# Optimization experiments

Measured on AMD Instinct MI355X. Metric: run time of the kernel, lower is better.

## Reference

```python
import jax, jax.numpy as jnp
import numpy as np
import itertools, math
from collections import Counter

# ----- circuit / state constants -----
M = 12            # modes
NPH = 5           # photons (input_state = [1]*5 + [0]*7)
NTHETA = 12       # trainable phase shifters
NX = 8            # input phase shifters (input_size)
NPARAMS = NTHETA + NX
OUT = 10
TWO_PI = 2.0 * np.pi

# all output Fock states with NPH photons in M modes, as sorted row-index multisets
ROW_IDX = np.array(list(itertools.combinations_with_replacement(range(M), NPH)), np.int32)  # [S, NPH]
S = ROW_IDX.shape[0]  # C(M+NPH-1, NPH) = 4368
# normalization prod(s_j!) for each output state (input state is 0/1 so its factor is 1)
NORM = np.array([np.prod([math.factorial(v) for v in Counter(tuple(r)).values()]) for r in ROW_IDX], np.float32)

# Ryser subsets of the NPH columns
K = 1 << NPH
MASKS = np.array([[(s >> j) & 1 for j in range(NPH)] for s in range(K)], np.float32)  # [K, NPH]
SIGNS = ((-1.0) ** (MASKS.sum(1) + NPH)).astype(np.float32)                            # [K]

# fixed 50/50 beamsplitter layers (perceval BS convention: 1/sqrt2 [[1, i],[i, 1]])
def _bs_layer(pairs):
    Bm = np.eye(M, dtype=np.complex64)
    r = np.float32(1.0 / np.sqrt(2.0))
    for (i, j) in pairs:
        Bm[i, i] = r; Bm[j, j] = r
        Bm[i, j] = 1j * r; Bm[j, i] = 1j * r
    return Bm
BS_EVEN = _bs_layer([(i, i + 1) for i in range(0, M - 1, 2)])
BS_ODD = _bs_layer([(i, i + 1) for i in range(1, M - 1, 2)])


def build_unitaries(x, thetas):
    """x: [B, NX] in [0,1]; thetas: [NTHETA]. Returns batched unitaries [B, M, M] complex64."""
    b = x.shape[0]
    phis = jnp.concatenate([jnp.broadcast_to(thetas, (b, NTHETA)), x * TWO_PI], axis=1)  # [B, NPARAMS]
    U = jnp.broadcast_to(jnp.eye(M, dtype=jnp.complex64), (b, M, M))
    for k in range(NPARAMS):
        mode = k % M
        phase = jnp.exp(1j * phis[:, k])  # [B] complex64
        ph = jnp.ones((b, M), jnp.complex64).at[:, mode].set(phase)
        U = ph[:, :, None] * U                               # apply phase shifter (diag @ U)
        Bm = jnp.asarray(BS_EVEN if k % 2 == 0 else BS_ODD)
        U = jnp.einsum('ij,bjk->bik', Bm, U)                 # apply BS layer
    return U


def slos_distribution(U):
    """Boson-sampling output distribution: p(s) = |perm(U[s_rows, :NPH])|^2 / prod(s_j!)."""
    Ucols = U[:, :, :NPH]  # photons enter modes 0..NPH-1 -> keep those columns, [B, M, NPH]
    masks = jnp.asarray(MASKS).astype(jnp.complex64)
    signs = jnp.asarray(SIGNS).astype(jnp.complex64)
    row_idx = jnp.asarray(ROW_IDX)

    def body(acc, ms):
        mask, sign = ms
        rs = Ucols @ mask              # row sums over subset columns, [B, M]
        rows = rs[:, row_idx]          # gather rows per output state, [B, S, NPH]
        return acc + sign * jnp.prod(rows, axis=-1), None

    acc0 = jnp.zeros((U.shape[0], S), jnp.complex64)
    perm, _ = jax.lax.scan(jax.checkpoint(body), acc0, (masks, signs))  # Ryser over 2^NPH subsets
    probs = (perm.real ** 2 + perm.imag ** 2) / jnp.asarray(NORM)
    return probs  # [B, S]


def setup_inputs() -> dict:
    key = jax.random.key(0)
    k1, k2, k3 = jax.random.split(key, 3)
    x = jax.random.uniform(k1, (512, NX), dtype=jnp.float32)                 # inputs in [0,1]
    thetas = jax.random.uniform(k2, (NTHETA,), dtype=jnp.float32) * np.pi    # init in [0, pi]
    W = jax.random.normal(k3, (S, OUT), dtype=jnp.float32) / np.sqrt(S)      # linear output mapping
    b = jnp.zeros((OUT,), jnp.float32)
    return {"x": x, "thetas": thetas, "W": W, "b": b}


def reference(x, thetas, W, b):
    U = build_unitaries(x, thetas)
    probs = slos_distribution(U)
    return probs @ W + b  # [B, OUT]
```

## Files before the change

kernel.cpp:

```cpp
#include <hip/hip_runtime.h>


#define MODES 12
#define NPH   5
#define KG    16
#define QG    8
#define NPAIR 78
#define S_TOT 4368
#define TPB   512
#define NWAVE (TPB / 64)
#define NOUT  10
#define NENT  720

#define TWO_PI_F 6.28318530717958647692f
#define RS2      0.70710678118654752440f

constexpr int Cnk(int n, int r) {
  int p = 1;
  for (int i = 0; i < r; ++i) p = p * (n - i) / (i + 1);
  return p;
}

struct Tables {
  unsigned       ea[NENT];
  unsigned       eb[NENT];
  unsigned char  wr[NENT];
  unsigned short cstart[TPB + 1];
  unsigned char  pairs[NPAIR];
};

constexpr Tables make_tables() {
  Tables T{};
  int ne = 0;
  for (int v = 11; v >= 0; --v) {
    unsigned P[364] = {};
    int cnt = 0;
    for (int m0 = 0; m0 <= v; ++m0)
      for (int m1 = m0; m1 <= v; ++m1)
        for (int m2 = m1; m2 <= v; ++m2) {
          int sbase = 0;
          for (int q = 0;  q < m0; ++q) sbase += Cnk(15 - q, 4);
          for (int q = m0; q < m1; ++q) sbase += Cnk(14 - q, 3);
          for (int q = m1; q < m2; ++q) sbase += Cnk(13 - q, 2);
          for (int q = m2; q < v;  ++q) sbase += 12 - q;
          int r1 = 1, pm = 1;
          r1 = (m1 == m0) ? r1 + 1 : 1; pm *= r1;
          r1 = (m2 == m1) ? r1 + 1 : 1; pm *= r1;
          r1 = (v  == m2) ? r1 + 1 : 1; pm *= r1;
          int code = 0;
          if (pm == 1)       code = 0;
          else if (pm == 2)  code = (r1 == 1) ? 1 : 2;
          else if (pm == 4)  code = 3;
          else if (pm == 6)  code = (r1 == 1) ? 4 : 5;
          else               code = 6;
          P[cnt++] = ((unsigned)code << 29) | ((unsigned)sbase << 16) |
                     ((unsigned)m0 << 12) | ((unsigned)m1 << 8) |
                     ((unsigned)m2 << 4) | (unsigned)v;
        }
    const int np = (cnt + 1) / 2;
    for (int j = 0; j < np; ++j) {
      unsigned a = P[2 * j];
      unsigned b = (2 * j + 1 < cnt) ? P[2 * j + 1] : a;
      if (v <= 4) {
        int mid = (v + 12) / 2;
        T.ea[ne] = a; T.eb[ne] = b; T.wr[ne] = (unsigned char)((v << 4) | mid);  ne++;
        T.ea[ne] = a; T.eb[ne] = b; T.wr[ne] = (unsigned char)((mid << 4) | 12); ne++;
      } else {
        T.ea[ne] = a; T.eb[ne] = b; T.wr[ne] = (unsigned char)((v << 4) | 12);   ne++;
      }
    }
  }
  long total = 0;
  for (int i = 0; i < NENT; ++i)
    total += 32 + 8 * ((T.wr[i] & 15) - (T.wr[i] >> 4));
  long cum = 0;
  int ci = 0;
  T.cstart[0] = 0;
  for (int i = 0; i < NENT; ++i) {
    cum += 32 + 8 * ((T.wr[i] & 15) - (T.wr[i] >> 4));
    while (ci < TPB - 1 && cum * TPB >= (long)(ci + 1) * total)
      T.cstart[++ci] = (unsigned short)(i + 1);
  }
  while (ci < TPB) T.cstart[++ci] = NENT;
  int pi = 0;
  for (int a = 0; a < MODES; ++a)
    for (int b = a; b < MODES; ++b)
      T.pairs[pi++] = (unsigned char)((a << 4) | b);
  return T;
}

__constant__ Tables g_tab = make_tables();

__constant__ float2 g_normlut[7] = {
  {1.f / 512.f,   1.f / 256.f},
  {1.f / 1024.f,  1.f / 512.f},
  {1.f / 1536.f,  1.f / 512.f},
  {1.f / 3072.f,  1.f / 1024.f},
  {1.f / 3072.f,  1.f / 1536.f},
  {1.f / 6144.f,  1.f / 1536.f},
  {1.f / 30720.f, 1.f / 6144.f},
};

#define BFLY(i, j)                                                 \
  { float ar = ur[i], ai = ui[i], br = ur[j], bi = ui[j];          \
    ur[i] = RS2 * (ar - bi); ui[i] = RS2 * (ai + br);              \
    ur[j] = RS2 * (br - ai); ui[j] = RS2 * (bi + ar); }

#define PREFA(q)                                                    \
  { float4 A = ppt[q][p01a], B = ppt[q][p2va];                      \
    pf##q = make_float4(A.x*B.x - A.y*B.y, A.x*B.y + A.y*B.x,       \
                        A.z*B.z - A.w*B.w, A.z*B.w + A.w*B.z); }
#define PREFB(q)                                                    \
  { float4 A = ppt[q][p01b], B = ppt[q][p2vb];                      \
    pg##q = make_float4(A.x*B.x - A.y*B.y, A.x*B.y + A.y*B.x,       \
                        A.z*B.z - A.w*B.w, A.z*B.w + A.w*B.z); }

#define WSTEP2(q, PRA, PIA, PRB, PIB)                                   \
  { float4 e2 = rsp[q][w];                                              \
    PRA = fmaf(pf##q.x, e2.x, PRA); PRA = fmaf(-pf##q.y, e2.y, PRA);    \
    PIA = fmaf(pf##q.x, e2.y, PIA); PIA = fmaf(pf##q.y, e2.x, PIA);     \
    PRA = fmaf(pf##q.z, e2.z, PRA); PRA = fmaf(-pf##q.w, e2.w, PRA);    \
    PIA = fmaf(pf##q.z, e2.w, PIA); PIA = fmaf(pf##q.w, e2.z, PIA);     \
    PRB = fmaf(pg##q.x, e2.x, PRB); PRB = fmaf(-pg##q.y, e2.y, PRB);    \
    PIB = fmaf(pg##q.x, e2.y, PIB); PIB = fmaf(pg##q.y, e2.x, PIB);     \
    PRB = fmaf(pg##q.z, e2.z, PRB); PRB = fmaf(-pg##q.w, e2.w, PRB);    \
    PIB = fmaf(pg##q.z, e2.w, PIB); PIB = fmaf(pg##q.w, e2.z, PIB); }

__global__ __launch_bounds__(TPB, 2) void qlayer_kernel(
    const float* __restrict__ x,
    const float* __restrict__ th,
    const float* __restrict__ W,
    const float* __restrict__ bias,
    float* __restrict__ out)
{
  __shared__ float4 rsp[QG][MODES];
  __shared__ float4 ppt[QG][NPAIR];
  __shared__ float  prob_lds[S_TOT];
  __shared__ float2 uc[MODES][NPH];
  __shared__ float2 sc[20];
  __shared__ float  wred[NWAVE][NOUT];

  const int b = blockIdx.x;
  const int t = threadIdx.x;

  if (t < 20) {
    float phi = (t < 12) ? th[t] : x[b * 8 + (t - 12)] * TWO_PI_F;
    float s, c;
    sincosf(phi, &s, &c);
    sc[t] = make_float2(s, c);
  }
  __syncthreads();

  if (t < NPH) {
    float ur[MODES], ui[MODES];
    #pragma unroll
    for (int m = 0; m < MODES; ++m) { ur[m] = 0.f; ui[m] = 0.f; }
    ur[t] = 1.f;
    #pragma unroll
    for (int k = 0; k < 20; ++k) {
      const int mode = k % MODES;
      float sp = sc[k].x, cp = sc[k].y;
      float re = ur[mode] * cp - ui[mode] * sp;
      float im = ur[mode] * sp + ui[mode] * cp;
      ur[mode] = re; ui[mode] = im;
      if ((k & 1) == 0) {
        BFLY(0, 1) BFLY(2, 3) BFLY(4, 5) BFLY(6, 7) BFLY(8, 9) BFLY(10, 11)
      } else {
        BFLY(1, 2) BFLY(3, 4) BFLY(5, 6) BFLY(7, 8) BFLY(9, 10)
      }
    }
    #pragma unroll
    for (int m = 0; m < MODES; ++m) uc[m][t] = make_float2(ur[m], ui[m]);
  }
  __syncthreads();

  if (t < QG * MODES) {
    const int q = t / MODES;
    const int m = t - q * MODES;
    const int k0 = 2 * q, k1 = 2 * q + 1;
    float r0 = uc[m][0].x, i0 = uc[m][0].y;
    float r1 = r0, i1 = i0;
    #pragma unroll
    for (int c = 1; c < NPH; ++c) {
      float ux = uc[m][c].x, uy = uc[m][c].y;
      float d0 = ((k0 >> (c - 1)) & 1) ? -1.f : 1.f;
      float d1 = ((k1 >> (c - 1)) & 1) ? -1.f : 1.f;
      r0 = fmaf(d0, ux, r0); i0 = fmaf(d0, uy, i0);
      r1 = fmaf(d1, ux, r1); i1 = fmaf(d1, uy, i1);
    }
    float sg0 = (__popc((unsigned)k0) & 1) ? -1.f : 1.f;
    float sg1 = (__popc((unsigned)k1) & 1) ? -1.f : 1.f;
    rsp[q][m] = make_float4(sg0 * r0, sg0 * i0, sg1 * r1, sg1 * i1);
  }
  __syncthreads();

  for (int i = t; i < QG * NPAIR; i += TPB) {
    const int q = i / NPAIR;
    const int p = i - q * NPAIR;
    const int ab = (int)g_tab.pairs[p];
    const int a = ab >> 4, b2 = ab & 15;
    float4 A = rsp[q][a], B = rsp[q][b2];
    ppt[q][p] = make_float4(A.x*B.x - A.y*B.y, A.x*B.y + A.y*B.x,
                            A.z*B.z - A.w*B.w, A.z*B.w + A.w*B.z);
  }
  __syncthreads();

  {
    const int beg = g_tab.cstart[t];
    const int end = g_tab.cstart[t + 1];
    for (int j = beg; j < end; ++j) {
      const unsigned eA = g_tab.ea[j];
      const unsigned eB = g_tab.eb[j];
      const int wrj = (int)g_tab.wr[j];
      const int w0 = wrj >> 4, w1 = wrj & 15;

      const int vA  = eA & 15;
      const int m2a = (eA >> 4) & 15, m1a = (eA >> 8) & 15, m0a = (eA >> 12) & 15;
      const int m2b = (eB >> 4) & 15, m1b = (eB >> 8) & 15, m0b = (eB >> 12) & 15;
      int siA = (int)((eA >> 16) & 0x1FFFu) + (w0 - vA);
      int siB = (int)((eB >> 16) & 0x1FFFu) + (w0 - vA);
      const float2 nlA = g_normlut[eA >> 29];
      const float2 nlB = g_normlut[eB >> 29];

      const int p01a = (m0a * (25 - m0a)) / 2 + (m1a - m0a);
      const int p2va = (m2a * (25 - m2a)) / 2 + (vA  - m2a);
      const int p01b = (m0b * (25 - m0b)) / 2 + (m1b - m0b);
      const int p2vb = (m2b * (25 - m2b)) / 2 + (vA  - m2b);

      float4 pf0, pf1, pf2, pf3, pf4, pf5, pf6, pf7;
      float4 pg0, pg1, pg2, pg3, pg4, pg5, pg6, pg7;
      PREFA(0) PREFA(1) PREFA(2) PREFA(3) PREFA(4) PREFA(5) PREFA(6) PREFA(7)
      PREFB(0) PREFB(1) PREFB(2) PREFB(3) PREFB(4) PREFB(5) PREFB(6) PREFB(7)

      float invnA = (w0 == vA) ? nlA.x : nlA.y;
      float invnB = (w0 == vA) ? nlB.x : nlB.y;
      for (int w = w0; w < w1; ++w, ++siA, ++siB) {
        float prA0 = 0.f, piA0 = 0.f, prA1 = 0.f, piA1 = 0.f;
        float prB0 = 0.f, piB0 = 0.f, prB1 = 0.f, piB1 = 0.f;
        WSTEP2(0, prA0, piA0, prB0, piB0) WSTEP2(1, prA0, piA0, prB0, piB0)
        WSTEP2(2, prA0, piA0, prB0, piB0) WSTEP2(3, prA0, piA0, prB0, piB0)
        WSTEP2(4, prA1, piA1, prB1, piB1) WSTEP2(5, prA1, piA1, prB1, piB1)
        WSTEP2(6, prA1, piA1, prB1, piB1) WSTEP2(7, prA1, piA1, prB1, piB1)
        float prA = prA0 + prA1, piA = piA0 + piA1;
        float prB = prB0 + prB1, piB = piB0 + piB1;
        prob_lds[siA] = (prA * prA + piA * piA) * invnA;
        prob_lds[siB] = (prB * prB + piB * piB) * invnB;
        invnA = nlA.y;
        invnB = nlB.y;
      }
    }
  }
  __syncthreads();

  float po[NOUT];
  #pragma unroll
  for (int o = 0; o < NOUT; ++o) po[o] = 0.f;

  const float2* __restrict__ W2 = (const float2*)W;
  #pragma unroll 2
  for (int r = 0; r < 8; ++r) {
    const int s = r * TPB + t;
    const float p = prob_lds[s];
    const float2* wr2 = W2 + (size_t)s * 5;
    float2 w01 = wr2[0], w23 = wr2[1], w45 = wr2[2], w67 = wr2[3], w89 = wr2[4];
    po[0] = fmaf(p, w01.x, po[0]); po[1] = fmaf(p, w01.y, po[1]);
    po[2] = fmaf(p, w23.x, po[2]); po[3] = fmaf(p, w23.y, po[3]);
    po[4] = fmaf(p, w45.x, po[4]); po[5] = fmaf(p, w45.y, po[5]);
    po[6] = fmaf(p, w67.x, po[6]); po[7] = fmaf(p, w67.y, po[7]);
    po[8] = fmaf(p, w89.x, po[8]); po[9] = fmaf(p, w89.y, po[9]);
  }
  if (t < S_TOT - 8 * TPB) {
    const int s = 8 * TPB + t;
    const float p = prob_lds[s];
    const float2* wr2 = W2 + (size_t)s * 5;
    float2 w01 = wr2[0], w23 = wr2[1], w45 = wr2[2], w67 = wr2[3], w89 = wr2[4];
    po[0] = fmaf(p, w01.x, po[0]); po[1] = fmaf(p, w01.y, po[1]);
    po[2] = fmaf(p, w23.x, po[2]); po[3] = fmaf(p, w23.y, po[3]);
    po[4] = fmaf(p, w45.x, po[4]); po[5] = fmaf(p, w45.y, po[5]);
    po[6] = fmaf(p, w67.x, po[6]); po[7] = fmaf(p, w67.y, po[7]);
    po[8] = fmaf(p, w89.x, po[8]); po[9] = fmaf(p, w89.y, po[9]);
  }

  #pragma unroll
  for (int o = 0; o < NOUT; ++o) {
    float v = po[o];
    #pragma unroll
    for (int off = 32; off > 0; off >>= 1) v += __shfl_down(v, off, 64);
    po[o] = v;
  }
  const int lane = t & 63, wave = t >> 6;
  if (lane == 0) {
    #pragma unroll
    for (int o = 0; o < NOUT; ++o) wred[wave][o] = po[o];
  }
  __syncthreads();
  if (t < NOUT) {
    float acc = bias[t];
    #pragma unroll
    for (int w2 = 0; w2 < NWAVE; ++w2) acc += wred[w2][t];
    out[b * NOUT + t] = acc;
  }
}

extern "C" void kernel_launch(void* const* d_in, const int* in_sizes, int n_in,
                              void* d_out, int out_size, void* d_ws, size_t ws_size,
                              hipStream_t stream) {
  (void)n_in; (void)out_size; (void)d_ws; (void)ws_size;
  const float* x    = (const float*)d_in[0];
  const float* th   = (const float*)d_in[1];
  const float* W    = (const float*)d_in[2];
  const float* bias = (const float*)d_in[3];
  float* out        = (float*)d_out;
  const int B = in_sizes[0] / 8;
  qlayer_kernel<<<B, TPB, 0, stream>>>(x, th, W, bias, out);
}
```

Measured before the change: 23.77 us.

## Parallelize unitary build across lanes, stage tables in LDS, fuse pair products

The 12x5 unitary columns are now built by 60 lanes, with phases and butterfly partners exchanged through wave shuffles, instead of 5 serial threads. Meanwhile the remaining threads copy the constant lookup tables (entries, widths, offsets, pairs, norms) into shared memory. The pair-product table is computed directly from the unitary columns, which removes one barrier stage at the cost of redundant row-sum arithmetic. The first W row is prefetched before the barrier so its latency overlaps the permanent loop.

```diff
diff --git a/kernel.cpp b/kernel.cpp
--- a/kernel.cpp
+++ b/kernel.cpp
@@ -101,11 +101,6 @@
   {1.f / 30720.f, 1.f / 6144.f},
 };
 
-#define BFLY(i, j)                                                 \
-  { float ar = ur[i], ai = ui[i], br = ur[j], bi = ui[j];          \
-    ur[i] = RS2 * (ar - bi); ui[i] = RS2 * (ai + br);              \
-    ur[j] = RS2 * (br - ai); ui[j] = RS2 * (bi + ar); }
-
 #define PREFA(q)                                                    \
   { float4 A = ppt[q][p01a], B = ppt[q][p2va];                      \
     pf##q = make_float4(A.x*B.x - A.y*B.y, A.x*B.y + A.y*B.x,       \
@@ -137,47 +132,71 @@
   __shared__ float4 ppt[QG][NPAIR];
   __shared__ float  prob_lds[S_TOT];
   __shared__ float2 uc[MODES][NPH];
-  __shared__ float2 sc[20];
   __shared__ float  wred[NWAVE][NOUT];
+  __shared__ unsigned       s_ea[NENT];
+  __shared__ unsigned       s_eb[NENT];
+  __shared__ unsigned char  s_wr[NENT];
+  __shared__ unsigned short s_cs[TPB + 1];
+  __shared__ unsigned char  s_pairs[NPAIR];
+  __shared__ float2         s_nl[7];
 
   const int b = blockIdx.x;
   const int t = threadIdx.x;
 
-  if (t < 20) {
-    float phi = (t < 12) ? th[t] : x[b * 8 + (t - 12)] * TWO_PI_F;
-    float s, c;
-    sincosf(phi, &s, &c);
-    sc[t] = make_float2(s, c);
-  }
-  __syncthreads();
-
-  if (t < NPH) {
-    float ur[MODES], ui[MODES];
-    #pragma unroll
-    for (int m = 0; m < MODES; ++m) { ur[m] = 0.f; ui[m] = 0.f; }
-    ur[t] = 1.f;
-    #pragma unroll
-    for (int k = 0; k < 20; ++k) {
-      const int mode = k % MODES;
-      float sp = sc[k].x, cp = sc[k].y;
-      float re = ur[mode] * cp - ui[mode] * sp;
-      float im = ur[mode] * sp + ui[mode] * cp;
-      ur[mode] = re; ui[mode] = im;
-      if ((k & 1) == 0) {
-        BFLY(0, 1) BFLY(2, 3) BFLY(4, 5) BFLY(6, 7) BFLY(8, 9) BFLY(10, 11)
-      } else {
-        BFLY(1, 2) BFLY(3, 4) BFLY(5, 6) BFLY(7, 8) BFLY(9, 10)
+  if (t < 64) {
+    float sp_own = 0.f, cp_own = 0.f;
+    if (t < 20) {
+      float phi = (t < 12) ? th[t] : x[b * 8 + (t - 12)] * TWO_PI_F;
+      sincosf(phi, &sp_own, &cp_own);
+    }
+    if (t < 60) {
+      const int col = t / 12, m = t - col * 12;
+      float re = (m == col) ? 1.f : 0.f, im = 0.f;
+      #pragma unroll
+      for (int k = 0; k < 20; ++k) {
+        const int mode = k % MODES;
+        float sp = __shfl(sp_own, k, 64);
+        float cp = __shfl(cp_own, k, 64);
+        float pre = re * cp - im * sp;
+        float pim = re * sp + im * cp;
+        re = (m == mode) ? pre : re;
+        im = (m == mode) ? pim : im;
+        int paired, pl;
+        if ((k & 1) == 0) {
+          paired = 1; pl = t ^ 1;
+        } else {
+          paired = (m >= 1 && m <= 10);
+          pl = paired ? (t - m + ((m & 1) ? m + 1 : m - 1)) : t;
+        }
+        float ore = __shfl(re, pl, 64);
+        float oim = __shfl(im, pl, 64);
+        if (paired) {
+          float nre = RS2 * (re - oim);
+          float nim = RS2 * (im + ore);
+          re = nre; im = nim;
+        }
       }
-    }
-    #pragma unroll
-    for (int m = 0; m < MODES; ++m) uc[m][t] = make_float2(ur[m], ui[m]);
+      uc[m][col] = make_float2(re, im);
+    }
+  } else {
+    for (int i = t - 64; i < NENT; i += TPB - 64) {
+      s_ea[i] = g_tab.ea[i];
+      s_eb[i] = g_tab.eb[i];
+      s_wr[i] = g_tab.wr[i];
+    }
+    for (int i = t - 64; i < TPB + 1; i += TPB - 64) s_cs[i] = g_tab.cstart[i];
+    if (t - 64 < NPAIR) s_pairs[t - 64] = g_tab.pairs[t - 64];
+    if (t == 64) {
+      #pragma unroll
+      for (int i = 0; i < 7; ++i) s_nl[i] = g_normlut[i];
+    }
   }
   __syncthreads();
 
   if (t < QG * MODES) {
     const int q = t / MODES;
     const int m = t - q * MODES;
-    const int k0 = 2 * q, k1 = 2 * q + 1;
+    const int k0 = 2 * q, k1 = k0 + 1;
     float r0 = uc[m][0].x, i0 = uc[m][0].y;
     float r1 = r0, i1 = i0;
     #pragma unroll
@@ -192,26 +211,42 @@
     float sg1 = (__popc((unsigned)k1) & 1) ? -1.f : 1.f;
     rsp[q][m] = make_float4(sg0 * r0, sg0 * i0, sg1 * r1, sg1 * i1);
   }
+  auto do_ppt = [&](int i) {
+    const int q = i / NPAIR, p = i - q * NPAIR;
+    const int ab = (int)s_pairs[p];
+    const int a = ab >> 4, b2 = ab & 15;
+    const int k0 = 2 * q, k1 = k0 + 1;
+    float ar0 = uc[a][0].x,  ai0 = uc[a][0].y,  ar1 = ar0, ai1 = ai0;
+    float br0 = uc[b2][0].x, bi0 = uc[b2][0].y, br1 = br0, bi1 = bi0;
+    #pragma unroll
+    for (int c = 1; c < NPH; ++c) {
+      float d0 = ((k0 >> (c - 1)) & 1) ? -1.f : 1.f;
+      float d1 = ((k1 >> (c - 1)) & 1) ? -1.f : 1.f;
+      float ux = uc[a][c].x,  uy = uc[a][c].y;
+      ar0 = fmaf(d0, ux, ar0); ai0 = fmaf(d0, uy, ai0);
+      ar1 = fmaf(d1, ux, ar1); ai1 = fmaf(d1, uy, ai1);
+      float vx = uc[b2][c].x, vy = uc[b2][c].y;
+      br0 = fmaf(d0, vx, br0); bi0 = fmaf(d0, vy, bi0);
+      br1 = fmaf(d1, vx, br1); bi1 = fmaf(d1, vy, bi1);
+    }
+    float sg0 = (__popc((unsigned)k0) & 1) ? -1.f : 1.f;
+    float sg1 = (__popc((unsigned)k1) & 1) ? -1.f : 1.f;
+    ar0 *= sg0; ai0 *= sg0; ar1 *= sg1; ai1 *= sg1;
+    br0 *= sg0; bi0 *= sg0; br1 *= sg1; bi1 *= sg1;
+    ppt[q][p] = make_float4(ar0 * br0 - ai0 * bi0, ar0 * bi0 + ai0 * br0,
+                            ar1 * br1 - ai1 * bi1, ar1 * bi1 + ai1 * br1);
+  };
+  do_ppt(t);
+  if (t >= 400) do_ppt(t + 112);
   __syncthreads();
 
-  for (int i = t; i < QG * NPAIR; i += TPB) {
-    const int q = i / NPAIR;
-    const int p = i - q * NPAIR;
-    const int ab = (int)g_tab.pairs[p];
-    const int a = ab >> 4, b2 = ab & 15;
-    float4 A = rsp[q][a], B = rsp[q][b2];
-    ppt[q][p] = make_float4(A.x*B.x - A.y*B.y, A.x*B.y + A.y*B.x,
-                            A.z*B.z - A.w*B.w, A.z*B.w + A.w*B.z);
-  }
-  __syncthreads();
-
   {
-    const int beg = g_tab.cstart[t];
-    const int end = g_tab.cstart[t + 1];
+    const int beg = s_cs[t];
+    const int end = s_cs[t + 1];
     for (int j = beg; j < end; ++j) {
-      const unsigned eA = g_tab.ea[j];
-      const unsigned eB = g_tab.eb[j];
-      const int wrj = (int)g_tab.wr[j];
+      const unsigned eA = s_ea[j];
+      const unsigned eB = s_eb[j];
+      const int wrj = (int)s_wr[j];
       const int w0 = wrj >> 4, w1 = wrj & 15;
 
       const int vA  = eA & 15;
@@ -219,8 +254,8 @@
       const int m2b = (eB >> 4) & 15, m1b = (eB >> 8) & 15, m0b = (eB >> 12) & 15;
       int siA = (int)((eA >> 16) & 0x1FFFu) + (w0 - vA);
       int siB = (int)((eB >> 16) & 0x1FFFu) + (w0 - vA);
-      const float2 nlA = g_normlut[eA >> 29];
-      const float2 nlB = g_normlut[eB >> 29];
+      const float2 nlA = s_nl[eA >> 29];
+      const float2 nlB = s_nl[eB >> 29];
 
       const int p01a = (m0a * (25 - m0a)) / 2 + (m1a - m0a);
       const int p2va = (m2a * (25 - m2a)) / 2 + (vA  - m2a);
@@ -250,15 +285,26 @@
       }
     }
   }
+
+  const float2* __restrict__ W2 = (const float2*)W;
+  const float2* wr0 = W2 + (size_t)t * 5;
+  float2 a01 = wr0[0], a23 = wr0[1], a45 = wr0[2], a67 = wr0[3], a89 = wr0[4];
   __syncthreads();
 
   float po[NOUT];
   #pragma unroll
   for (int o = 0; o < NOUT; ++o) po[o] = 0.f;
 
-  const float2* __restrict__ W2 = (const float2*)W;
+  {
+    const float p = prob_lds[t];
+    po[0] = fmaf(p, a01.x, po[0]); po[1] = fmaf(p, a01.y, po[1]);
+    po[2] = fmaf(p, a23.x, po[2]); po[3] = fmaf(p, a23.y, po[3]);
+    po[4] = fmaf(p, a45.x, po[4]); po[5] = fmaf(p, a45.y, po[5]);
+    po[6] = fmaf(p, a67.x, po[6]); po[7] = fmaf(p, a67.y, po[7]);
+    po[8] = fmaf(p, a89.x, po[8]); po[9] = fmaf(p, a89.y, po[9]);
+  }
   #pragma unroll 2
-  for (int r = 0; r < 8; ++r) {
+  for (int r = 1; r < 8; ++r) {
     const int s = r * TPB + t;
     const float p = prob_lds[s];
     const float2* wr2 = W2 + (size_t)s * 5;
```

New measurement: 21.77 us. 1.09x faster.
